# Optimization experiments

Measured on AMD Instinct MI355X. Metric: run time of the kernel, lower is better.

Reference implementation:

```python
import jax, jax.numpy as jnp
import numpy as np

N_NODES, D_H, D_MSG, N_LAYERS = 512, 64, 64, 3
T, E = 128, 8192


def setup_inputs() -> dict:
    key = jax.random.key(0)
    ks = jax.random.split(key, 16)
    s = 0.1
    t = jax.random.uniform(ks[0], (T,), dtype=jnp.float32)
    edge_index = jax.random.randint(ks[1], (2, E), 0, N_NODES, dtype=jnp.int64)
    inp = {
        "t": t,
        "edge_index": edge_index,
        "enc_w": jax.random.normal(ks[2], (1 + N_NODES, D_H), jnp.float32) * s,
        "enc_b": jnp.zeros((D_H,), jnp.float32),
        "msg1_w": jax.random.normal(ks[3], (N_LAYERS, 2 * D_H, D_MSG), jnp.float32) * s,
        "msg1_b": jnp.zeros((N_LAYERS, D_MSG), jnp.float32),
        "msg2_w": jax.random.normal(ks[4], (N_LAYERS, D_MSG, D_MSG), jnp.float32) * s,
        "msg2_b": jnp.zeros((N_LAYERS, D_MSG), jnp.float32),
        "upd1_w": jax.random.normal(ks[5], (N_LAYERS, D_H + D_MSG, D_H), jnp.float32) * s,
        "upd1_b": jnp.zeros((N_LAYERS, D_H), jnp.float32),
        "upd2_w": jax.random.normal(ks[6], (N_LAYERS, D_H, D_H), jnp.float32) * s,
        "upd2_b": jnp.zeros((N_LAYERS, D_H), jnp.float32),
        "ro_w": jax.random.normal(ks[7], (D_H, 1), jnp.float32) * s,
        "ro_b": jnp.zeros((1,), jnp.float32),
    }
    return inp


def reference(t, edge_index, enc_w, enc_b, msg1_w, msg1_b, msg2_w, msg2_b,
              upd1_w, upd1_b, upd2_w, upd2_b, ro_w, ro_b):
    Tn = t.shape[0]
    N = enc_w.shape[0] - 1
    L = msg1_w.shape[0]
    # node features: [t, one_hot(node_id)] -> encode
    t_feat = jnp.broadcast_to(t[:, None, None], (Tn, N, 1))          # [T,N,1]
    id_feat = jnp.broadcast_to(jnp.eye(N, dtype=t.dtype), (Tn, N, N))  # [T,N,N]
    x = jnp.concatenate([t_feat, id_feat], axis=-1)                   # [T,N,1+N]
    h = x @ enc_w + enc_b                                             # [T,N,d_h]
    src, dst = edge_index[0], edge_index[1]
    for l in range(L):
        # message MLP on gathered [h_src, h_dst]
        cat = jnp.concatenate([h[:, src], h[:, dst]], axis=-1)        # [T,E,2*d_h]
        m = jax.nn.silu(cat @ msg1_w[l] + msg1_b[l]) @ msg2_w[l] + msg2_b[l]  # [T,E,d_msg]
        # scatter-add into destination nodes (index_add)
        agg = jnp.zeros((Tn, N, m.shape[-1]), dtype=h.dtype).at[:, dst].add(m)
        u = jnp.concatenate([h, agg], axis=-1)                        # [T,N,d_h+d_msg]
        upd = jax.nn.silu(u @ upd1_w[l] + upd1_b[l]) @ upd2_w[l] + upd2_b[l]
        h = h + upd                                                   # residual
    out = (h @ ro_w + ro_b)[..., 0]                                   # [T,N]
    return out
```

## Files before the change

kernel.cpp:

```cpp
#include <hip/hip_runtime.h>

#define TT 128
#define NN 512
#define DH 64
#define EE 8192
#define LOB (18 * 8 * 64)

typedef __bf16 bf16x8 __attribute__((ext_vector_type(8)));
typedef float f32x4 __attribute__((ext_vector_type(4)));

struct US8 { unsigned short u[8]; };
struct Frag { bf16x8 hi, lo; };

static __device__ __forceinline__ unsigned short f2bf(float x) {
    union { float f; unsigned u; } c; c.f = x;
    unsigned r = (c.u + 0x7FFFu + ((c.u >> 16) & 1u)) >> 16;
    return (unsigned short)r;
}
static __device__ __forceinline__ float bf2f(unsigned short b) {
    union { unsigned u; float f; } c; c.u = ((unsigned)b) << 16;
    return c.f;
}
static __device__ __forceinline__ float silu_acc(float a, float b, float acc) {
    float x = a + b;
    float e = __expf(-x);
    return fmaf(x, __builtin_amdgcn_rcpf(1.0f + e), acc);
}
static __device__ __forceinline__ float silu_f(float x) {
    float e = __expf(-x);
    return x * __builtin_amdgcn_rcpf(1.0f + e);
}
static __device__ __forceinline__ Frag split8(const float* v) {
    Frag f;
    #pragma unroll
    for (int i = 0; i < 8; ++i) {
        __bf16 hb = (__bf16)v[i];
        f.hi[i] = hb;
        f.lo[i] = (__bf16)(v[i] - (float)hb);
    }
    return f;
}
static __device__ __forceinline__ f32x4 mmac(bf16x8 a, uint4 bw, f32x4 c) {
    return __builtin_amdgcn_mfma_f32_16x16x32_bf16(
        a, __builtin_bit_cast(bf16x8, bw), c, 0, 0, 0);
}
static __device__ __forceinline__ f32x4 mm3(Frag a, uint4 wh, uint4 wl, f32x4 c) {
    c = mmac(a.hi, wh, c);
    c = mmac(a.lo, wh, c);
    c = mmac(a.hi, wl, c);
    return c;
}

__global__ __launch_bounds__(512) void setup_kernel(
    const int* __restrict__ ei,
    const float* __restrict__ msg1_w, const float* __restrict__ msg2_w,
    const float* __restrict__ upd1_w, const float* __restrict__ upd2_w,
    uint4* __restrict__ pack,
    int* __restrict__ counts, int* __restrict__ offsets,
    int* __restrict__ ssrc) {
    int b = blockIdx.x;
    if (b < 18) {
        int l = b / 6, bi = b % 6;
        const float* W;
        if (bi == 0)      W = msg1_w + (size_t)l * 128 * 64;
        else if (bi == 1) W = msg1_w + (size_t)l * 128 * 64 + 64 * 64;
        else if (bi == 2) W = msg2_w + (size_t)l * 64 * 64;
        else if (bi == 3) W = upd1_w + (size_t)l * 128 * 64;
        else if (bi == 4) W = upd1_w + (size_t)l * 128 * 64 + 64 * 64;
        else              W = upd2_w + (size_t)l * 64 * 64;
        int lane = threadIdx.x & 63;
        int sub  = threadIdx.x >> 6;
        int nt = sub >> 1, kc = sub & 1;
        US8 oh, ol;
        #pragma unroll
        for (int i = 0; i < 8; ++i) {
            int k = kc * 32 + (lane >> 4) * 8 + i;
            int col = nt * 16 + (lane & 15);
            float w = W[k * 64 + col];
            unsigned short hu = f2bf(w);
            oh.u[i] = hu;
            ol.u[i] = f2bf(w - bf2f(hu));
        }
        size_t fi = ((size_t)b * 8 + sub) * 64 + lane;
        pack[fi]       = __builtin_bit_cast(uint4, oh);
        pack[LOB + fi] = __builtin_bit_cast(uint4, ol);
        return;
    }
    __shared__ int cnt[NN];
    __shared__ int tmp[NN];
    __shared__ int cur[NN];
    int i = threadIdx.x;
    cnt[i] = 0;
    __syncthreads();
    #pragma unroll
    for (int r = 0; r < EE / 512; ++r)
        atomicAdd(&cnt[ei[EE + r * 512 + i]], 1);
    __syncthreads();
    int c = cnt[i];
    tmp[i] = c;
    __syncthreads();
    for (int off = 1; off < NN; off <<= 1) {
        int v = (i >= off) ? tmp[i - off] : 0;
        __syncthreads();
        tmp[i] += v;
        __syncthreads();
    }
    counts[i] = c;
    offsets[i + 1] = tmp[i];
    if (i == 0) offsets[0] = 0;
    cur[i] = tmp[i] - c;
    __syncthreads();
    #pragma unroll
    for (int r = 0; r < EE / 512; ++r) {
        int e = r * 512 + i;
        int dst = ei[EE + e];
        int pos = atomicAdd(&cur[dst], 1);
        ssrc[pos] = ei[e];
    }
}

static __device__ __forceinline__ int swz_rowbase(int bid, int w) {
    int xcd = bid & 7;
    int idx = bid >> 3;
    int tt  = xcd * 16 + (idx >> 3);
    int sub = idx & 7;
    return tt * NN + sub * 64 + w * 16;
}

__global__ __launch_bounds__(256) void encode_mfma_kernel(
    const float* __restrict__ t, const float* __restrict__ enc_w,
    const float* __restrict__ enc_b, const float* __restrict__ b1,
    const uint4* __restrict__ pack,
    float* __restrict__ h, float* __restrict__ hs, float* __restrict__ hd) {
    int lane = threadIdx.x & 63;
    int rowbase = swz_rowbase(blockIdx.x, threadIdx.x >> 6);
    int arow = lane & 15, kgrp = lane >> 4, k0 = kgrp * 8;
    int row = rowbase + arow;
    int tt = row >> 9, n = row & (NN - 1);
    float tv = t[tt];

    float hv[16];
    #pragma unroll
    for (int kc = 0; kc < 2; ++kc) {
        #pragma unroll
        for (int i = 0; i < 8; ++i) {
            int k = kc * 32 + k0 + i;
            hv[kc * 8 + i] = tv * enc_w[k] + enc_w[(1 + n) * DH + k] + enc_b[k];
        }
        *(float4*)(h + (size_t)row * DH + kc * 32 + k0) =
            make_float4(hv[kc * 8], hv[kc * 8 + 1], hv[kc * 8 + 2], hv[kc * 8 + 3]);
        *(float4*)(h + (size_t)row * DH + kc * 32 + k0 + 4) =
            make_float4(hv[kc * 8 + 4], hv[kc * 8 + 5], hv[kc * 8 + 6], hv[kc * 8 + 7]);
    }
    Frag a0 = split8(&hv[0]), a1 = split8(&hv[8]);

    const uint4* PWtH = pack;
    const uint4* PWbH = pack + 8 * 64;
    const uint4* PWtL = PWtH + LOB;
    const uint4* PWbL = PWbH + LOB;
    #pragma unroll
    for (int nt = 0; nt < 4; ++nt) {
        f32x4 s; f32x4 d;
        float b1v = b1[nt * 16 + (lane & 15)];
        #pragma unroll
        for (int r = 0; r < 4; ++r) { s[r] = 0.f; d[r] = b1v; }
        s = mm3(a0, PWtH[(nt * 2 + 0) * 64 + lane], PWtL[(nt * 2 + 0) * 64 + lane], s);
        s = mm3(a1, PWtH[(nt * 2 + 1) * 64 + lane], PWtL[(nt * 2 + 1) * 64 + lane], s);
        d = mm3(a0, PWbH[(nt * 2 + 0) * 64 + lane], PWbL[(nt * 2 + 0) * 64 + lane], d);
        d = mm3(a1, PWbH[(nt * 2 + 1) * 64 + lane], PWbL[(nt * 2 + 1) * 64 + lane], d);
        #pragma unroll
        for (int r = 0; r < 4; ++r) {
            int rr = rowbase + kgrp * 4 + r;
            hs[(size_t)rr * DH + nt * 16 + (lane & 15)] = s[r];
            hd[(size_t)rr * DH + nt * 16 + (lane & 15)] = d[r];
        }
    }
}

__global__ __launch_bounds__(256) void agg_kernel(
    const float* __restrict__ hs, const float* __restrict__ hd,
    const int* __restrict__ offsets, const int* __restrict__ ssrc,
    float* __restrict__ aggpre) {
    int bid = blockIdx.x;
    int xcd = bid & 7;
    int idx = bid >> 3;
    int tt  = xcd * 16 + (idx >> 7);
    int n   = (idx & 127) * 4 + (threadIdx.x >> 6);
    int lane = threadIdx.x & 63;
    size_t rowoff = ((size_t)tt * NN + n) * DH;
    int eg = lane >> 4;
    int ch4 = (lane & 15) * 16;
    float4 hdv = *(const float4*)(hd + rowoff + (lane & 15) * 4);
    int beg = offsets[n], end = offsets[n + 1];
    const char* hb = (const char*)(hs + (size_t)tt * NN * DH);
    float4 acc = make_float4(0.f, 0.f, 0.f, 0.f);
    int i = beg + eg;
    for (; i + 4 < end; i += 8) {
        int s0 = ssrc[i] << 8;
        int s1 = ssrc[i + 4] << 8;
        float4 v0 = *(const float4*)(hb + s0 + ch4);
        float4 v1 = *(const float4*)(hb + s1 + ch4);
        acc.x = silu_acc(v0.x, hdv.x, acc.x);
        acc.y = silu_acc(v0.y, hdv.y, acc.y);
        acc.z = silu_acc(v0.z, hdv.z, acc.z);
        acc.w = silu_acc(v0.w, hdv.w, acc.w);
        acc.x = silu_acc(v1.x, hdv.x, acc.x);
        acc.y = silu_acc(v1.y, hdv.y, acc.y);
        acc.z = silu_acc(v1.z, hdv.z, acc.z);
        acc.w = silu_acc(v1.w, hdv.w, acc.w);
    }
    if (i < end) {
        int s0 = ssrc[i] << 8;
        float4 v0 = *(const float4*)(hb + s0 + ch4);
        acc.x = silu_acc(v0.x, hdv.x, acc.x);
        acc.y = silu_acc(v0.y, hdv.y, acc.y);
        acc.z = silu_acc(v0.z, hdv.z, acc.z);
        acc.w = silu_acc(v0.w, hdv.w, acc.w);
    }
    acc.x += __shfl_xor(acc.x, 16); acc.x += __shfl_xor(acc.x, 32);
    acc.y += __shfl_xor(acc.y, 16); acc.y += __shfl_xor(acc.y, 32);
    acc.z += __shfl_xor(acc.z, 16); acc.z += __shfl_xor(acc.z, 32);
    acc.w += __shfl_xor(acc.w, 16); acc.w += __shfl_xor(acc.w, 32);
    if (eg == 0) *(float4*)(aggpre + rowoff + (lane & 15) * 4) = acc;
}

__global__ __launch_bounds__(256) void upd_mfma_kernel(
    float* __restrict__ h, const float* __restrict__ aggpre,
    const int* __restrict__ counts, const uint4* __restrict__ pack, int l,
    const float* __restrict__ b2, const float* __restrict__ ub1,
    const float* __restrict__ ub2, const float* __restrict__ b1n,
    float* __restrict__ hs, float* __restrict__ hd,
    const float* __restrict__ ro_w, const float* __restrict__ ro_b,
    float* __restrict__ out, int last) {
    __shared__ float tile[4][16 * 68];
    int lane = threadIdx.x & 63;
    int w = threadIdx.x >> 6;
    int rowbase = swz_rowbase(blockIdx.x, w);
    float* TA = tile[w];
    int arow = lane & 15, kgrp = lane >> 4, k0 = kgrp * 8;
    int hrow = rowbase + arow;

    float hf[16];
    *(float4*)&hf[0]  = *(const float4*)(h + (size_t)hrow * DH + k0);
    *(float4*)&hf[4]  = *(const float4*)(h + (size_t)hrow * DH + k0 + 4);
    *(float4*)&hf[8]  = *(const float4*)(h + (size_t)hrow * DH + 32 + k0);
    *(float4*)&hf[12] = *(const float4*)(h + (size_t)hrow * DH + 32 + k0 + 4);
    Frag ha0 = split8(&hf[0]), ha1 = split8(&hf[8]);

    float gf[16];
    *(float4*)&gf[0]  = *(const float4*)(aggpre + (size_t)hrow * DH + k0);
    *(float4*)&gf[4]  = *(const float4*)(aggpre + (size_t)hrow * DH + k0 + 4);
    *(float4*)&gf[8]  = *(const float4*)(aggpre + (size_t)hrow * DH + 32 + k0);
    *(float4*)&gf[12] = *(const float4*)(aggpre + (size_t)hrow * DH + 32 + k0 + 4);
    Frag ga0 = split8(&gf[0]), ga1 = split8(&gf[8]);

    const uint4* PW2H = pack + (size_t)(l * 6 + 2) * 8 * 64;
    const uint4* PW2L = PW2H + LOB;
    float degv[4];
    #pragma unroll
    for (int r = 0; r < 4; ++r)
        degv[r] = (float)counts[(rowbase + kgrp * 4 + r) & (NN - 1)];
    #pragma unroll
    for (int nt = 0; nt < 4; ++nt) {
        float b2v = b2[nt * 16 + (lane & 15)];
        f32x4 a;
        #pragma unroll
        for (int r = 0; r < 4; ++r) a[r] = degv[r] * b2v;
        a = mm3(ga0, PW2H[(nt * 2 + 0) * 64 + lane], PW2L[(nt * 2 + 0) * 64 + lane], a);
        a = mm3(ga1, PW2H[(nt * 2 + 1) * 64 + lane], PW2L[(nt * 2 + 1) * 64 + lane], a);
        #pragma unroll
        for (int r = 0; r < 4; ++r)
            TA[(kgrp * 4 + r) * 68 + nt * 16 + (lane & 15)] = a[r];
    }
    float za[16];
    #pragma unroll
    for (int i = 0; i < 8; ++i) za[i] = TA[arow * 68 + k0 + i];
    #pragma unroll
    for (int i = 0; i < 8; ++i) za[8 + i] = TA[arow * 68 + 32 + k0 + i];
    Frag ka0 = split8(&za[0]), ka1 = split8(&za[8]);

    const uint4* PU1tH = pack + (size_t)(l * 6 + 3) * 8 * 64;
    const uint4* PU1bH = pack + (size_t)(l * 6 + 4) * 8 * 64;
    const uint4* PU1tL = PU1tH + LOB;
    const uint4* PU1bL = PU1bH + LOB;
    #pragma unroll
    for (int nt = 0; nt < 4; ++nt) {
        float bv = ub1[nt * 16 + (lane & 15)];
        f32x4 a;
        #pragma unroll
        for (int r = 0; r < 4; ++r) a[r] = bv;
        a = mm3(ha0, PU1tH[(nt * 2 + 0) * 64 + lane], PU1tL[(nt * 2 + 0) * 64 + lane], a);
        a = mm3(ha1, PU1tH[(nt * 2 + 1) * 64 + lane], PU1tL[(nt * 2 + 1) * 64 + lane], a);
        a = mm3(ka0, PU1bH[(nt * 2 + 0) * 64 + lane], PU1bL[(nt * 2 + 0) * 64 + lane], a);
        a = mm3(ka1, PU1bH[(nt * 2 + 1) * 64 + lane], PU1bL[(nt * 2 + 1) * 64 + lane], a);
        #pragma unroll
        for (int r = 0; r < 4; ++r)
            TA[(kgrp * 4 + r) * 68 + nt * 16 + (lane & 15)] = silu_f(a[r]);
    }
    float zb[16];
    #pragma unroll
    for (int i = 0; i < 8; ++i) zb[i] = TA[arow * 68 + k0 + i];
    #pragma unroll
    for (int i = 0; i < 8; ++i) zb[8 + i] = TA[arow * 68 + 32 + k0 + i];
    Frag kz0 = split8(&zb[0]), kz1 = split8(&zb[8]);

    const uint4* PU2H = pack + (size_t)(l * 6 + 5) * 8 * 64;
    const uint4* PU2L = PU2H + LOB;
    #pragma unroll
    for (int nt = 0; nt < 4; ++nt) {
        float bv = ub2[nt * 16 + (lane & 15)];
        f32x4 a;
        #pragma unroll
        for (int r = 0; r < 4; ++r) a[r] = bv;
        a = mm3(kz0, PU2H[(nt * 2 + 0) * 64 + lane], PU2L[(nt * 2 + 0) * 64 + lane], a);
        a = mm3(kz1, PU2H[(nt * 2 + 1) * 64 + lane], PU2L[(nt * 2 + 1) * 64 + lane], a);
        #pragma unroll
        for (int r = 0; r < 4; ++r)
            TA[(kgrp * 4 + r) * 68 + nt * 16 + (lane & 15)] = a[r];
    }
    float hn[16];
    #pragma unroll
    for (int i = 0; i < 8; ++i) hn[i] = hf[i] + TA[arow * 68 + k0 + i];
    #pragma unroll
    for (int i = 0; i < 8; ++i) hn[8 + i] = hf[8 + i] + TA[arow * 68 + 32 + k0 + i];

    if (last) {
        float v = 0.f;
        #pragma unroll
        for (int i = 0; i < 8; ++i) v += hn[i] * ro_w[k0 + i];
        #pragma unroll
        for (int i = 0; i < 8; ++i) v += hn[8 + i] * ro_w[32 + k0 + i];
        v += __shfl_xor(v, 16);
        v += __shfl_xor(v, 32);
        if (lane < 16) out[rowbase + lane] = v + ro_b[0];
        return;
    }

    *(float4*)(h + (size_t)hrow * DH + k0) = make_float4(hn[0], hn[1], hn[2], hn[3]);
    *(float4*)(h + (size_t)hrow * DH + k0 + 4) = make_float4(hn[4], hn[5], hn[6], hn[7]);
    *(float4*)(h + (size_t)hrow * DH + 32 + k0) = make_float4(hn[8], hn[9], hn[10], hn[11]);
    *(float4*)(h + (size_t)hrow * DH + 32 + k0 + 4) = make_float4(hn[12], hn[13], hn[14], hn[15]);

    Frag na0 = split8(&hn[0]), na1 = split8(&hn[8]);
    const uint4* PWtH = pack + (size_t)((l + 1) * 6 + 0) * 8 * 64;
    const uint4* PWbH = pack + (size_t)((l + 1) * 6 + 1) * 8 * 64;
    const uint4* PWtL = PWtH + LOB;
    const uint4* PWbL = PWbH + LOB;
    #pragma unroll
    for (int nt = 0; nt < 4; ++nt) {
        f32x4 s; f32x4 d;
        float b1v = b1n[nt * 16 + (lane & 15)];
        #pragma unroll
        for (int r = 0; r < 4; ++r) { s[r] = 0.f; d[r] = b1v; }
        s = mm3(na0, PWtH[(nt * 2 + 0) * 64 + lane], PWtL[(nt * 2 + 0) * 64 + lane], s);
        s = mm3(na1, PWtH[(nt * 2 + 1) * 64 + lane], PWtL[(nt * 2 + 1) * 64 + lane], s);
        d = mm3(na0, PWbH[(nt * 2 + 0) * 64 + lane], PWbL[(nt * 2 + 0) * 64 + lane], d);
        d = mm3(na1, PWbH[(nt * 2 + 1) * 64 + lane], PWbL[(nt * 2 + 1) * 64 + lane], d);
        #pragma unroll
        for (int r = 0; r < 4; ++r) {
            int rr = rowbase + kgrp * 4 + r;
            hs[(size_t)rr * DH + nt * 16 + (lane & 15)] = s[r];
            hd[(size_t)rr * DH + nt * 16 + (lane & 15)] = d[r];
        }
    }
}

extern "C" void kernel_launch(void* const* d_in, const int* in_sizes, int n_in,
                              void* d_out, int out_size, void* d_ws, size_t ws_size,
                              hipStream_t stream) {
    const float* t      = (const float*)d_in[0];
    const int*   ei     = (const int*)d_in[1];
    const float* enc_w  = (const float*)d_in[2];
    const float* enc_b  = (const float*)d_in[3];
    const float* msg1_w = (const float*)d_in[4];
    const float* msg1_b = (const float*)d_in[5];
    const float* msg2_w = (const float*)d_in[6];
    const float* msg2_b = (const float*)d_in[7];
    const float* upd1_w = (const float*)d_in[8];
    const float* upd1_b = (const float*)d_in[9];
    const float* upd2_w = (const float*)d_in[10];
    const float* upd2_b = (const float*)d_in[11];
    const float* ro_w   = (const float*)d_in[12];
    const float* ro_b   = (const float*)d_in[13];
    float* out = (float*)d_out;

    const size_t HN = (size_t)TT * NN * DH;
    float* h      = (float*)d_ws;
    float* hs     = h + HN;
    float* hd     = hs + HN;
    float* aggpre = hd + HN;
    uint4* pack   = (uint4*)(aggpre + HN);
    int* counts  = (int*)(pack + 2 * LOB);
    int* offsets = counts + NN;
    int* ssrc    = offsets + NN + 1;

    setup_kernel<<<19, 512, 0, stream>>>(ei, msg1_w, msg2_w, upd1_w, upd2_w,
                                         pack, counts, offsets, ssrc);

    encode_mfma_kernel<<<TT * NN / 64, 256, 0, stream>>>(
        t, enc_w, enc_b, msg1_b, pack, h, hs, hd);

    for (int l = 0; l < 3; ++l) {
        agg_kernel<<<TT * NN / 4, 256, 0, stream>>>(
            hs, hd, offsets, ssrc, aggpre);
        int last = (l == 2);
        upd_mfma_kernel<<<TT * NN / 64, 256, 0, stream>>>(
            h, aggpre, counts, pack, l,
            msg2_b + (size_t)l * DH, upd1_b + (size_t)l * DH,
            upd2_b + (size_t)l * DH,
            last ? msg1_b : msg1_b + (size_t)(l + 1) * DH,
            hs, hd, ro_w, ro_b, out, last);
    }
}
```

Measured before the change: 275.5 us.

## Fold encoder into layer-0 message projection and drop encode kernel

Since the encoded node state is affine in t, the layer-0 message-MLP first projection is precomputed per node (E1s, E1d) plus a t-coefficient vector in the setup kernel. A new agg0 kernel gathers these small node-only tables instead of per-timestep hs/hd, and the layer-0 update kernel recomputes h from the encoder weights on the fly. This removes the encode kernel and its full h/hs/hd writes, at the cost of extra setup blocks doing fp32 dot products and a different rounding path from the split-bf16 MFMA version.

```diff
diff --git a/kernel.cpp b/kernel.cpp
--- a/kernel.cpp
+++ b/kernel.cpp
@@ -55,9 +55,13 @@
     const int* __restrict__ ei,
     const float* __restrict__ msg1_w, const float* __restrict__ msg2_w,
     const float* __restrict__ upd1_w, const float* __restrict__ upd2_w,
+    const float* __restrict__ enc_w, const float* __restrict__ enc_b,
+    const float* __restrict__ msg1_b,
     uint4* __restrict__ pack,
     int* __restrict__ counts, int* __restrict__ offsets,
-    int* __restrict__ ssrc) {
+    int* __restrict__ ssrc,
+    float* __restrict__ E1s, float* __restrict__ E1d,
+    float* __restrict__ e0sum) {
     int b = blockIdx.x;
     if (b < 18) {
         int l = b / 6, bi = b % 6;
@@ -86,36 +90,64 @@
         pack[LOB + fi] = __builtin_bit_cast(uint4, ol);
         return;
     }
-    __shared__ int cnt[NN];
-    __shared__ int tmp[NN];
-    __shared__ int cur[NN];
-    int i = threadIdx.x;
-    cnt[i] = 0;
-    __syncthreads();
-    #pragma unroll
-    for (int r = 0; r < EE / 512; ++r)
-        atomicAdd(&cnt[ei[EE + r * 512 + i]], 1);
-    __syncthreads();
-    int c = cnt[i];
-    tmp[i] = c;
-    __syncthreads();
-    for (int off = 1; off < NN; off <<= 1) {
-        int v = (i >= off) ? tmp[i - off] : 0;
+    if (b == 18) {
+        __shared__ int cnt[NN];
+        __shared__ int tmp[NN];
+        __shared__ int cur[NN];
+        int i = threadIdx.x;
+        cnt[i] = 0;
         __syncthreads();
-        tmp[i] += v;
+        #pragma unroll
+        for (int r = 0; r < EE / 512; ++r)
+            atomicAdd(&cnt[ei[EE + r * 512 + i]], 1);
         __syncthreads();
-    }
-    counts[i] = c;
-    offsets[i + 1] = tmp[i];
-    if (i == 0) offsets[0] = 0;
-    cur[i] = tmp[i] - c;
-    __syncthreads();
-    #pragma unroll
-    for (int r = 0; r < EE / 512; ++r) {
-        int e = r * 512 + i;
-        int dst = ei[EE + e];
-        int pos = atomicAdd(&cur[dst], 1);
-        ssrc[pos] = ei[e];
+        int c = cnt[i];
+        tmp[i] = c;
+        __syncthreads();
+        for (int off = 1; off < NN; off <<= 1) {
+            int v = (i >= off) ? tmp[i - off] : 0;
+            __syncthreads();
+            tmp[i] += v;
+            __syncthreads();
+        }
+        counts[i] = c;
+        offsets[i + 1] = tmp[i];
+        if (i == 0) offsets[0] = 0;
+        cur[i] = tmp[i] - c;
+        __syncthreads();
+        #pragma unroll
+        for (int r = 0; r < EE / 512; ++r) {
+            int e = r * 512 + i;
+            int dst = ei[EE + e];
+            int pos = atomicAdd(&cur[dst], 1);
+            ssrc[pos] = ei[e];
+        }
+        return;
+    }
+    if (b < 83) {
+        int nn = (b - 19) * 8 + (threadIdx.x >> 6);
+        int d  = threadIdx.x & 63;
+        float s = 0.f, dd = msg1_b[d];
+        #pragma unroll 8
+        for (int k = 0; k < 64; ++k) {
+            float c = enc_w[(1 + nn) * 64 + k] + enc_b[k];
+            s  = fmaf(c, msg1_w[k * 64 + d], s);
+            dd = fmaf(c, msg1_w[(64 + k) * 64 + d], dd);
+        }
+        E1s[nn * 64 + d] = s;
+        E1d[nn * 64 + d] = dd;
+        return;
+    }
+    if (threadIdx.x < 64) {
+        int d = threadIdx.x;
+        float s = 0.f, dd = 0.f;
+        #pragma unroll 8
+        for (int k = 0; k < 64; ++k) {
+            float a = enc_w[k];
+            s  = fmaf(a, msg1_w[k * 64 + d], s);
+            dd = fmaf(a, msg1_w[(64 + k) * 64 + d], dd);
+        }
+        e0sum[d] = s + dd;
     }
 }
 
@@ -127,54 +159,57 @@
     return tt * NN + sub * 64 + w * 16;
 }
 
-__global__ __launch_bounds__(256) void encode_mfma_kernel(
-    const float* __restrict__ t, const float* __restrict__ enc_w,
-    const float* __restrict__ enc_b, const float* __restrict__ b1,
-    const uint4* __restrict__ pack,
-    float* __restrict__ h, float* __restrict__ hs, float* __restrict__ hd) {
+__global__ __launch_bounds__(256) void agg0_kernel(
+    const float* __restrict__ t, const float* __restrict__ e0sum,
+    const float* __restrict__ E1s, const float* __restrict__ E1d,
+    const int* __restrict__ offsets, const int* __restrict__ ssrc,
+    float* __restrict__ aggpre) {
+    int bid = blockIdx.x;
+    int xcd = bid & 7;
+    int idx = bid >> 3;
+    int tt  = xcd * 16 + (idx >> 7);
+    int n   = (idx & 127) * 4 + (threadIdx.x >> 6);
     int lane = threadIdx.x & 63;
-    int rowbase = swz_rowbase(blockIdx.x, threadIdx.x >> 6);
-    int arow = lane & 15, kgrp = lane >> 4, k0 = kgrp * 8;
-    int row = rowbase + arow;
-    int tt = row >> 9, n = row & (NN - 1);
+    int eg = lane >> 4;
+    int chb = (lane & 15) * 4;
+    int ch4 = chb * 4;
     float tv = t[tt];
-
-    float hv[16];
-    #pragma unroll
-    for (int kc = 0; kc < 2; ++kc) {
-        #pragma unroll
-        for (int i = 0; i < 8; ++i) {
-            int k = kc * 32 + k0 + i;
-            hv[kc * 8 + i] = tv * enc_w[k] + enc_w[(1 + n) * DH + k] + enc_b[k];
-        }
-        *(float4*)(h + (size_t)row * DH + kc * 32 + k0) =
-            make_float4(hv[kc * 8], hv[kc * 8 + 1], hv[kc * 8 + 2], hv[kc * 8 + 3]);
-        *(float4*)(h + (size_t)row * DH + kc * 32 + k0 + 4) =
-            make_float4(hv[kc * 8 + 4], hv[kc * 8 + 5], hv[kc * 8 + 6], hv[kc * 8 + 7]);
-    }
-    Frag a0 = split8(&hv[0]), a1 = split8(&hv[8]);
-
-    const uint4* PWtH = pack;
-    const uint4* PWbH = pack + 8 * 64;
-    const uint4* PWtL = PWtH + LOB;
-    const uint4* PWbL = PWbH + LOB;
-    #pragma unroll
-    for (int nt = 0; nt < 4; ++nt) {
-        f32x4 s; f32x4 d;
-        float b1v = b1[nt * 16 + (lane & 15)];
-        #pragma unroll
-        for (int r = 0; r < 4; ++r) { s[r] = 0.f; d[r] = b1v; }
-        s = mm3(a0, PWtH[(nt * 2 + 0) * 64 + lane], PWtL[(nt * 2 + 0) * 64 + lane], s);
-        s = mm3(a1, PWtH[(nt * 2 + 1) * 64 + lane], PWtL[(nt * 2 + 1) * 64 + lane], s);
-        d = mm3(a0, PWbH[(nt * 2 + 0) * 64 + lane], PWbL[(nt * 2 + 0) * 64 + lane], d);
-        d = mm3(a1, PWbH[(nt * 2 + 1) * 64 + lane], PWbL[(nt * 2 + 1) * 64 + lane], d);
-        #pragma unroll
-        for (int r = 0; r < 4; ++r) {
-            int rr = rowbase + kgrp * 4 + r;
-            hs[(size_t)rr * DH + nt * 16 + (lane & 15)] = s[r];
-            hd[(size_t)rr * DH + nt * 16 + (lane & 15)] = d[r];
-        }
-    }
+    float4 e0 = *(const float4*)(e0sum + chb);
+    float4 ed = *(const float4*)(E1d + n * DH + chb);
+    float4 base = make_float4(fmaf(tv, e0.x, ed.x), fmaf(tv, e0.y, ed.y),
+                              fmaf(tv, e0.z, ed.z), fmaf(tv, e0.w, ed.w));
+    int beg = offsets[n], end = offsets[n + 1];
+    const char* Eb = (const char*)E1s;
+    float4 acc = make_float4(0.f, 0.f, 0.f, 0.f);
+    int i = beg + eg;
+    for (; i + 4 < end; i += 8) {
+        int s0 = ssrc[i] << 8;
+        int s1 = ssrc[i + 4] << 8;
+        float4 v0 = *(const float4*)(Eb + s0 + ch4);
+        float4 v1 = *(const float4*)(Eb + s1 + ch4);
+        acc.x = silu_acc(v0.x, base.x, acc.x);
+        acc.y = silu_acc(v0.y, base.y, acc.y);
+        acc.z = silu_acc(v0.z, base.z, acc.z);
+        acc.w = silu_acc(v0.w, base.w, acc.w);
+        acc.x = silu_acc(v1.x, base.x, acc.x);
+        acc.y = silu_acc(v1.y, base.y, acc.y);
+        acc.z = silu_acc(v1.z, base.z, acc.z);
+        acc.w = silu_acc(v1.w, base.w, acc.w);
+    }
+    if (i < end) {
+        int s0 = ssrc[i] << 8;
+        float4 v0 = *(const float4*)(Eb + s0 + ch4);
+        acc.x = silu_acc(v0.x, base.x, acc.x);
+        acc.y = silu_acc(v0.y, base.y, acc.y);
+        acc.z = silu_acc(v0.z, base.z, acc.z);
+        acc.w = silu_acc(v0.w, base.w, acc.w);
+    }
+    acc.x += __shfl_xor(acc.x, 16); acc.x += __shfl_xor(acc.x, 32);
+    acc.y += __shfl_xor(acc.y, 16); acc.y += __shfl_xor(acc.y, 32);
+    acc.z += __shfl_xor(acc.z, 16); acc.z += __shfl_xor(acc.z, 32);
+    acc.w += __shfl_xor(acc.w, 16); acc.w += __shfl_xor(acc.w, 32);
+    if (eg == 0)
+        *(float4*)(aggpre + ((size_t)tt * NN + n) * DH + chb) = acc;
 }
 
 __global__ __launch_bounds__(256) void agg_kernel(
@@ -226,12 +261,14 @@
 
 __global__ __launch_bounds__(256) void upd_mfma_kernel(
     float* __restrict__ h, const float* __restrict__ aggpre,
+    const float* __restrict__ t, const float* __restrict__ enc_w,
+    const float* __restrict__ enc_b,
     const int* __restrict__ counts, const uint4* __restrict__ pack, int l,
     const float* __restrict__ b2, const float* __restrict__ ub1,
     const float* __restrict__ ub2, const float* __restrict__ b1n,
     float* __restrict__ hs, float* __restrict__ hd,
     const float* __restrict__ ro_w, const float* __restrict__ ro_b,
-    float* __restrict__ out, int last) {
+    float* __restrict__ out, int first, int last) {
     __shared__ float tile[4][16 * 68];
     int lane = threadIdx.x & 63;
     int w = threadIdx.x >> 6;
@@ -241,10 +278,22 @@
     int hrow = rowbase + arow;
 
     float hf[16];
-    *(float4*)&hf[0]  = *(const float4*)(h + (size_t)hrow * DH + k0);
-    *(float4*)&hf[4]  = *(const float4*)(h + (size_t)hrow * DH + k0 + 4);
-    *(float4*)&hf[8]  = *(const float4*)(h + (size_t)hrow * DH + 32 + k0);
-    *(float4*)&hf[12] = *(const float4*)(h + (size_t)hrow * DH + 32 + k0 + 4);
+    if (first) {
+        int n = (rowbase & (NN - 1)) + arow;
+        float tv = t[rowbase >> 9];
+        #pragma unroll
+        for (int kc = 0; kc < 2; ++kc)
+            #pragma unroll
+            for (int i = 0; i < 8; ++i) {
+                int k = kc * 32 + k0 + i;
+                hf[kc * 8 + i] = tv * enc_w[k] + enc_w[(1 + n) * DH + k] + enc_b[k];
+            }
+    } else {
+        *(float4*)&hf[0]  = *(const float4*)(h + (size_t)hrow * DH + k0);
+        *(float4*)&hf[4]  = *(const float4*)(h + (size_t)hrow * DH + k0 + 4);
+        *(float4*)&hf[8]  = *(const float4*)(h + (size_t)hrow * DH + 32 + k0);
+        *(float4*)&hf[12] = *(const float4*)(h + (size_t)hrow * DH + 32 + k0 + 4);
+    }
     Frag ha0 = split8(&hf[0]), ha1 = split8(&hf[8]);
 
     float gf[16];
@@ -254,7 +303,7 @@
     *(float4*)&gf[12] = *(const float4*)(aggpre + (size_t)hrow * DH + 32 + k0 + 4);
     Frag ga0 = split8(&gf[0]), ga1 = split8(&gf[8]);
 
-    const uint4* PW2H = pack + (size_t)(l * 6 + 2) * 8 * 64;
+    const uint4* PW2H = pack + (size_t)(l * 6 + 2) * 512;
     const uint4* PW2L = PW2H + LOB;
     float degv[4];
     #pragma unroll
@@ -279,8 +328,8 @@
     for (int i = 0; i < 8; ++i) za[8 + i] = TA[arow * 68 + 32 + k0 + i];
     Frag ka0 = split8(&za[0]), ka1 = split8(&za[8]);
 
-    const uint4* PU1tH = pack + (size_t)(l * 6 + 3) * 8 * 64;
-    const uint4* PU1bH = pack + (size_t)(l * 6 + 4) * 8 * 64;
+    const uint4* PU1tH = pack + (size_t)(l * 6 + 3) * 512;
+    const uint4* PU1bH = pack + (size_t)(l * 6 + 4) * 512;
     const uint4* PU1tL = PU1tH + LOB;
     const uint4* PU1bL = PU1bH + LOB;
     #pragma unroll
@@ -304,7 +353,7 @@
     for (int i = 0; i < 8; ++i) zb[8 + i] = TA[arow * 68 + 32 + k0 + i];
     Frag kz0 = split8(&zb[0]), kz1 = split8(&zb[8]);
 
-    const uint4* PU2H = pack + (size_t)(l * 6 + 5) * 8 * 64;
+    const uint4* PU2H = pack + (size_t)(l * 6 + 5) * 512;
     const uint4* PU2L = PU2H + LOB;
     #pragma unroll
     for (int nt = 0; nt < 4; ++nt) {
@@ -342,8 +391,8 @@
     *(float4*)(h + (size_t)hrow * DH + 32 + k0 + 4) = make_float4(hn[12], hn[13], hn[14], hn[15]);
 
     Frag na0 = split8(&hn[0]), na1 = split8(&hn[8]);
-    const uint4* PWtH = pack + (size_t)((l + 1) * 6 + 0) * 8 * 64;
-    const uint4* PWbH = pack + (size_t)((l + 1) * 6 + 1) * 8 * 64;
+    const uint4* PWtH = pack + (size_t)((l + 1) * 6 + 0) * 512;
+    const uint4* PWbH = pack + (size_t)((l + 1) * 6 + 1) * 512;
     const uint4* PWtL = PWtH + LOB;
     const uint4* PWbL = PWbH + LOB;
     #pragma unroll
@@ -393,22 +442,28 @@
     int* counts  = (int*)(pack + 2 * LOB);
     int* offsets = counts + NN;
     int* ssrc    = offsets + NN + 1;
-
-    setup_kernel<<<19, 512, 0, stream>>>(ei, msg1_w, msg2_w, upd1_w, upd2_w,
-                                         pack, counts, offsets, ssrc);
-
-    encode_mfma_kernel<<<TT * NN / 64, 256, 0, stream>>>(
-        t, enc_w, enc_b, msg1_b, pack, h, hs, hd);
+    float* E1s   = (float*)(ssrc + EE);
+    float* E1d   = E1s + NN * DH;
+    float* e0sum = E1d + NN * DH;
+
+    setup_kernel<<<84, 512, 0, stream>>>(ei, msg1_w, msg2_w, upd1_w, upd2_w,
+                                         enc_w, enc_b, msg1_b,
+                                         pack, counts, offsets, ssrc,
+                                         E1s, E1d, e0sum);
 
     for (int l = 0; l < 3; ++l) {
-        agg_kernel<<<TT * NN / 4, 256, 0, stream>>>(
-            hs, hd, offsets, ssrc, aggpre);
+        if (l == 0)
+            agg0_kernel<<<TT * NN / 4, 256, 0, stream>>>(
+                t, e0sum, E1s, E1d, offsets, ssrc, aggpre);
+        else
+            agg_kernel<<<TT * NN / 4, 256, 0, stream>>>(
+                hs, hd, offsets, ssrc, aggpre);
         int last = (l == 2);
         upd_mfma_kernel<<<TT * NN / 64, 256, 0, stream>>>(
-            h, aggpre, counts, pack, l,
+            h, aggpre, t, enc_w, enc_b, counts, pack, l,
             msg2_b + (size_t)l * DH, upd1_b + (size_t)l * DH,
             upd2_b + (size_t)l * DH,
             last ? msg1_b : msg1_b + (size_t)(l + 1) * DH,
-            hs, hd, ro_w, ro_b, out, last);
-    }
-}
+            hs, hd, ro_w, ro_b, out, (l == 0) ? 1 : 0, last);
+    }
+}
```

After: 247.2 us, median of 2. -10.3%, faster.
